# Performance work log

Measured on AMD Instinct MI355X. Metric: run time of the kernel, lower is better.

## Reference

```python
import jax, jax.numpy as jnp
import numpy as np

NUM_HEADS = 8
SPLIT = 2  # split_size; idx=0 -> H_sp=H, W_sp=SPLIT (horizontal stripes)


def setup_inputs() -> dict:
    key = jax.random.key(0)
    k1, k2, k3 = jax.random.split(key, 3)
    B, C, H, W = 4, 64, 128, 128
    temp = jax.random.normal(k1, (B, 3, C, H, W), dtype=jnp.float32)
    conv_w = jax.random.normal(k2, (C, 1, 3, 3), dtype=jnp.float32) * 0.1  # depthwise OIHW
    conv_b = jax.random.normal(k3, (C,), dtype=jnp.float32) * 0.1
    return {"temp": temp, "conv_w": conv_w, "conv_b": conv_b}


def reference(temp, conv_w, conv_b):
    B, _, C, H, W = temp.shape
    hd = C // NUM_HEADS
    scale = hd ** (-0.5)
    H_sp, W_sp = H, SPLIT  # idx == 0

    # symmetric pad to multiples of window size (faithful to original; zero here)
    H_pad = (H_sp - H % H_sp) % H_sp
    W_pad = (W_sp - W % W_sp) % W_sp
    top, left = H_pad // 2, W_pad // 2
    x = jnp.pad(temp, ((0, 0), (0, 0), (0, 0), (top, H_pad - top), (left, W_pad - left)))
    H_, W_ = H + H_pad, W + W_pad
    q, k, v = x[:, 0], x[:, 1], x[:, 2]  # each [B,C,H_,W_]

    nW = (H_ // H_sp) * (W_ // W_sp)
    N = H_sp * W_sp  # tokens per window

    def im2cswin(t):
        # [B,C,H_,W_] -> [B*nW, heads, N, hd]
        w = t.reshape(B, C, H_ // H_sp, H_sp, W_ // W_sp, W_sp)
        w = w.transpose(0, 2, 4, 3, 5, 1).reshape(-1, N, C)
        return w.reshape(-1, N, NUM_HEADS, hd).transpose(0, 2, 1, 3)

    qh = im2cswin(q) * scale
    kh = im2cswin(k)

    # v windows as images [B*nW, C, H_sp, W_sp] for depthwise LePE conv
    vw = v.reshape(B, C, H_ // H_sp, H_sp, W_ // W_sp, W_sp)
    vw = vw.transpose(0, 2, 4, 1, 3, 5).reshape(-1, C, H_sp, W_sp)
    rpe = jax.lax.conv_general_dilated(
        vw, conv_w, window_strides=(1, 1), padding='SAME',
        feature_group_count=C, dimension_numbers=('NCHW', 'OIHW', 'NCHW'))
    rpe = rpe + conv_b[None, :, None, None]

    vh = vw.reshape(-1, NUM_HEADS, hd, N).transpose(0, 1, 3, 2)    # [B*nW,h,N,hd]
    rpeh = rpe.reshape(-1, NUM_HEADS, hd, N).transpose(0, 1, 3, 2)

    attn = jax.nn.softmax(jnp.einsum('whnd,whmd->whnm', qh, kh), axis=-1)
    out = jnp.einsum('whnm,whmd->whnd', attn, vh) + rpeh           # [B*nW,h,N,hd]

    out = out.transpose(0, 2, 1, 3).reshape(-1, N, C)              # [B*nW,N,C]
    # windows2img + crop
    out = out.reshape(B, H_ // H_sp, W_ // W_sp, H_sp, W_sp, C)
    out = out.transpose(0, 1, 3, 2, 4, 5).reshape(B, H_, W_, C)
    out = out[:, top:H + top, left:W + left, :]
    return out.reshape(B, H * W, C)
```

## Files before the change

### kernel.cpp

```cpp
#include <hip/hip_runtime.h>
#include <hip/hip_bf16.h>
#include <stdint.h>


typedef __attribute__((ext_vector_type(4))) short bf16x4;
typedef __attribute__((ext_vector_type(4))) float f32x4;

static __device__ __forceinline__ uint32_t pk2(float x, float y) {
    union { __hip_bfloat162 h2; uint32_t u; } c;
    c.h2 = __float22bfloat162_rn(make_float2(x, y));
    return c.u;
}
static __device__ __forceinline__ float bflo(uint32_t u){ return __uint_as_float(u<<16); }
static __device__ __forceinline__ float bfhi(uint32_t u){ return __uint_as_float(u & 0xffff0000u); }

static __device__ __forceinline__ uint2 ld2(const char* p) {
    uint2 r;
    r.x = *(const uint32_t*)(p);
    r.y = *(const uint32_t*)(p + 4);
    return r;
}

static __device__ __forceinline__ int qk_off(int tok) {
    return (tok * 16) ^ ((tok >> 4 & 7) << 4);
}

static __device__ __forceinline__ f32x4 mfma16x16x16bf16(bf16x4 a, bf16x4 b, f32x4 c) {
#if __has_builtin(__builtin_amdgcn_mfma_f32_16x16x16bf16_1k)
    return __builtin_amdgcn_mfma_f32_16x16x16bf16_1k(a, b, c, 0, 0, 0);
#else
    f32x4 d;
    asm volatile("v_mfma_f32_16x16x16_bf16 %0, %1, %2, %3\n\ts_nop 7\n\ts_nop 7"
                 : "=v"(d) : "v"(a), "v"(b), "v"(c));
    return d;
#endif
}

#define QK_WIN_STR 4128
#define V_CH_STR   536
#define V_WIN_STR  4288

__global__ __launch_bounds__(256, 4)
void lepe_attn(const float* __restrict__ temp,
               const float* __restrict__ conv_w,
               const float* __restrict__ conv_b,
               float* __restrict__ out)
{
    __shared__ __align__(16) char smem[25408];
    char* q_s = smem;
    char* k_s = smem + 8256;
    char* v_t = smem + 16512;
    float* cw_s = (float*)(smem + 25088);

    const int tid  = threadIdx.x;
    const int wave = tid >> 6, lane = tid & 63;
    const int lr = lane & 15, quad = lane >> 4;
    const int win   = wave & 1;
    const int qbase = (wave >> 1) * 8;

    const int bid = blockIdx.x;
    const int x  = bid & 7;
    int t_ = bid >> 3;
    const int wq   = t_ & 3;  t_ >>= 2;
    const int head = t_ & 7;
    const int b    = t_ >> 3;
    const int wi   = x*8 + wq*2 + win;

    const size_t cstr = 16384, sstr = 64 * cstr;
    const float qs = 0.35355339059327373f * 1.4426950408889634f;

    {
        #pragma unroll
        for (int i = 0; i < 4; ++i) {
            int r  = i*256 + tid;
            int ch = r >> 7;
            int h  = r & 127;
            const float* bp = temp + (size_t)b*3*sstr + (size_t)(head*8 + ch)*cstr
                            + (size_t)h*128 + x*16 + wq*4;
            int o0 = qk_off(2*h), o1 = qk_off(2*h + 1);
            float4 fq = *(const float4*)(bp);
            uint32_t a0 = pk2(fq.x*qs, fq.y*qs);
            uint32_t a1 = pk2(fq.z*qs, fq.w*qs);
            *(uint16_t*)(q_s + o0 + ch*2)              = (uint16_t)a0;
            *(uint16_t*)(q_s + o1 + ch*2)              = (uint16_t)(a0>>16);
            *(uint16_t*)(q_s + QK_WIN_STR + o0 + ch*2) = (uint16_t)a1;
            *(uint16_t*)(q_s + QK_WIN_STR + o1 + ch*2) = (uint16_t)(a1>>16);
            float4 fk = *(const float4*)(bp + sstr);
            uint32_t b0 = pk2(fk.x, fk.y);
            uint32_t b1 = pk2(fk.z, fk.w);
            *(uint16_t*)(k_s + o0 + ch*2)              = (uint16_t)b0;
            *(uint16_t*)(k_s + o1 + ch*2)              = (uint16_t)(b0>>16);
            *(uint16_t*)(k_s + QK_WIN_STR + o0 + ch*2) = (uint16_t)b1;
            *(uint16_t*)(k_s + QK_WIN_STR + o1 + ch*2) = (uint16_t)(b1>>16);
            float4 fv = *(const float4*)(bp + 2*sstr);
            *(uint32_t*)(v_t + ch*V_CH_STR + 4*h + 4)             = pk2(fv.x, fv.y);
            *(uint32_t*)(v_t + V_WIN_STR + ch*V_CH_STR + 4*h + 4) = pk2(fv.z, fv.w);
        }
        if (tid < 72) cw_s[tid] = conv_w[head*72 + tid];
        if (tid < 8)  cw_s[72 + tid] = conv_b[head*8 + tid];
        if (tid < 16) {
            int vw = tid >> 3, vc = tid & 7;
            *(uint32_t*)(v_t + vw*V_WIN_STR + vc*V_CH_STR)       = 0;
            *(uint32_t*)(v_t + vw*V_WIN_STR + vc*V_CH_STR + 516) = 0;
        }
    }
    __syncthreads();

    const f32x4 zf = {0.f, 0.f, 0.f, 0.f};
    const uint2 z2 = make_uint2(0, 0);
    const uint2 ones2 = make_uint2(0x3F803F80u, 0x3F803F80u);
    uint2 kf[16]; uint2 vf[16];
    #pragma unroll
    for (int T = 0; T < 16; ++T) {
        uint2 kk = ld2(k_s + win*QK_WIN_STR + qk_off(T*16 + lr) + (quad & 1)*8);
        kf[T] = (quad < 2) ? kk : z2;
        uint2 vv = ld2(v_t + win*V_WIN_STR + (lane & 7)*V_CH_STR + 4 + (T*16 + quad*4)*2);
        vf[T] = (lr < 8) ? vv : ((lr == 8) ? ones2 : z2);
    }
    __syncthreads();

    {
        const int w2  = tid >> 7;
        const int chl = (tid >> 4) & 7;
        const int seg = tid & 15;
        const char* base = v_t + w2*V_WIN_STR + chl*V_CH_STR + seg*32;
        uint32_t d[10];
        *(uint2*)(d+0) = *(const uint2*)(base);
        *(uint2*)(d+2) = *(const uint2*)(base+8);
        *(uint2*)(d+4) = *(const uint2*)(base+16);
        *(uint2*)(d+6) = *(const uint2*)(base+24);
        *(uint2*)(d+8) = *(const uint2*)(base+32);
        float w9[9];
        #pragma unroll
        for (int k = 0; k < 9; ++k) w9[k] = cw_s[chl*9 + k];
        const float bia = cw_s[72 + chl];
        #pragma unroll
        for (int tt = 0; tt < 16; ++tt) {
            int tok = seg*16 + tt;
            int w01 = tok & 1;
            int L = (tt >> 1) * 2;
            float rp = bia;
            #pragma unroll
            for (int dy = 0; dy < 3; ++dy) {
                #pragma unroll
                for (int wp = 0; wp < 2; ++wp) {
                    int idx = L + 2*dy + wp;
                    uint32_t dw = d[idx >> 1];
                    float tap = (idx & 1) ? bfhi(dw) : bflo(dw);
                    rp = fmaf(w9[dy*3 + wp + 1 - w01], tap, rp);
                }
            }
            union { __hip_bfloat16 h; uint16_t u; } cv;
            cv.h = __float2bfloat16(rp);
            *(uint16_t*)(k_s + w2*QK_WIN_STR + qk_off(tok) + chl*2) = cv.u;
        }
    }
    __syncthreads();

    #pragma unroll 1
    for (int qg0 = 0; qg0 < 8; ++qg0) {
        const int qg = qbase + qg0;
        uint2 qq = ld2(q_s + win*QK_WIN_STR + qk_off(qg*16 + lr) + (quad & 1)*8);
        union { uint2 u; bf16x4 h4; } qf; qf.u = (quad < 2) ? qq : z2;
        f32x4 acc0 = zf, acc1 = zf;
        #pragma unroll
        for (int T = 0; T < 16; T += 2) {
            union { uint2 u; bf16x4 h4; } kfu0; kfu0.u = kf[T];
            union { uint2 u; bf16x4 h4; } kfu1; kfu1.u = kf[T+1];
            f32x4 sc0 = mfma16x16x16bf16(kfu0.h4, qf.h4, zf);
            f32x4 sc1 = mfma16x16x16bf16(kfu1.h4, qf.h4, zf);
            float a0 = __builtin_amdgcn_exp2f(sc0[0]);
            float a1 = __builtin_amdgcn_exp2f(sc0[1]);
            float a2 = __builtin_amdgcn_exp2f(sc0[2]);
            float a3 = __builtin_amdgcn_exp2f(sc0[3]);
            float b0_ = __builtin_amdgcn_exp2f(sc1[0]);
            float b1_ = __builtin_amdgcn_exp2f(sc1[1]);
            float b2_ = __builtin_amdgcn_exp2f(sc1[2]);
            float b3_ = __builtin_amdgcn_exp2f(sc1[3]);
            union { uint2 u; bf16x4 h4; } pb0; pb0.u = make_uint2(pk2(a0,a1), pk2(a2,a3));
            union { uint2 u; bf16x4 h4; } pb1; pb1.u = make_uint2(pk2(b0_,b1_), pk2(b2_,b3_));
            union { uint2 u; bf16x4 h4; } vf0; vf0.u = vf[T];
            union { uint2 u; bf16x4 h4; } vf1; vf1.u = vf[T+1];
            acc0 = mfma16x16x16bf16(vf0.h4, pb0.h4, acc0);
            acc1 = mfma16x16x16bf16(vf1.h4, pb1.h4, acc1);
        }
        f32x4 acc;
        acc[0] = acc0[0] + acc1[0];
        acc[1] = acc0[1] + acc1[1];
        acc[2] = acc0[2] + acc1[2];
        acc[3] = acc0[3] + acc1[3];
        float rs = __shfl(acc[0], 32 + lr);
        const float rinv = __builtin_amdgcn_rcpf(rs);
        if (quad < 2) {
            int tok = qg*16 + lr;
            int h = tok >> 1, w01 = tok & 1;
            uint2 rp2 = ld2(k_s + win*QK_WIN_STR + qk_off(tok) + quad*8);
            float4 ov;
            ov.x = fmaf(acc[0], rinv, bflo(rp2.x));
            ov.y = fmaf(acc[1], rinv, bfhi(rp2.x));
            ov.z = fmaf(acc[2], rinv, bflo(rp2.y));
            ov.w = fmaf(acc[3], rinv, bfhi(rp2.y));
            size_t addr = (size_t)b*1048576 + (size_t)(h*128 + wi*2 + w01)*64
                        + head*8 + quad*4;
            *(float4*)(out + addr) = ov;
        }
    }
}

extern "C" void kernel_launch(void* const* d_in, const int* in_sizes, int n_in,
                              void* d_out, int out_size, void* d_ws, size_t ws_size,
                              hipStream_t stream) {
    const float* temp = (const float*)d_in[0];
    const float* cw   = (const float*)d_in[1];
    const float* cb   = (const float*)d_in[2];
    float* o = (float*)d_out;
    (void)in_sizes; (void)n_in; (void)out_size; (void)d_ws; (void)ws_size;
    lepe_attn<<<dim3(1024), dim3(256), 0, stream>>>(temp, cw, cb, o);
}
```

Baseline: 112.8 us.

## Process eight windows per 1024-thread block for coalesced input loads

Each block now covers all eight stripe windows of a 16-column slab with 1024 threads and 100 KB of LDS, instead of two windows with 256 threads. Four consecutive threads read 64 contiguous bytes of a row, replacing the earlier 16-byte fragments, so global read coalescing should improve. The grid shrinks to 256 blocks, which allows only one block per CU because of the LDS size, and barriers now span 16 waves. The launch bound of 1024 threads with 4 blocks may also push the compiler into a tight register cap, which risks spilling the kf/vf fragment arrays.

```diff
diff --git a/kernel.cpp b/kernel.cpp
--- a/kernel.cpp
+++ b/kernel.cpp
@@ -40,65 +40,66 @@
 #define V_CH_STR   536
 #define V_WIN_STR  4288
 
-__global__ __launch_bounds__(256, 4)
+__global__ __launch_bounds__(1024, 4)
 void lepe_attn(const float* __restrict__ temp,
                const float* __restrict__ conv_w,
                const float* __restrict__ conv_b,
                float* __restrict__ out)
 {
-    __shared__ __align__(16) char smem[25408];
+    __shared__ __align__(16) char smem[100672];
     char* q_s = smem;
-    char* k_s = smem + 8256;
-    char* v_t = smem + 16512;
-    float* cw_s = (float*)(smem + 25088);
+    char* k_s = smem + 33024;
+    char* v_t = smem + 66048;
+    float* cw_s = (float*)(smem + 100352);
 
     const int tid  = threadIdx.x;
     const int wave = tid >> 6, lane = tid & 63;
     const int lr = lane & 15, quad = lane >> 4;
-    const int win   = wave & 1;
-    const int qbase = (wave >> 1) * 8;
+    const int win   = wave & 7;
+    const int qbase = (wave >> 3) * 8;
 
     const int bid = blockIdx.x;
-    const int x  = bid & 7;
+    const int x    = bid & 7;
     int t_ = bid >> 3;
-    const int wq   = t_ & 3;  t_ >>= 2;
     const int head = t_ & 7;
     const int b    = t_ >> 3;
-    const int wi   = x*8 + wq*2 + win;
+    const int wi   = x*8 + win;
 
     const size_t cstr = 16384, sstr = 64 * cstr;
     const float qs = 0.35355339059327373f * 1.4426950408889634f;
 
     {
+        const int chunk = tid & 3;
+        const int h     = (tid >> 2) & 127;
+        const int chp   = tid >> 9;
+        const int w0    = chunk * 2;
         #pragma unroll
         for (int i = 0; i < 4; ++i) {
-            int r  = i*256 + tid;
-            int ch = r >> 7;
-            int h  = r & 127;
+            int ch = i*2 + chp;
             const float* bp = temp + (size_t)b*3*sstr + (size_t)(head*8 + ch)*cstr
-                            + (size_t)h*128 + x*16 + wq*4;
+                            + (size_t)h*128 + x*16 + chunk*4;
             int o0 = qk_off(2*h), o1 = qk_off(2*h + 1);
             float4 fq = *(const float4*)(bp);
             uint32_t a0 = pk2(fq.x*qs, fq.y*qs);
             uint32_t a1 = pk2(fq.z*qs, fq.w*qs);
-            *(uint16_t*)(q_s + o0 + ch*2)              = (uint16_t)a0;
-            *(uint16_t*)(q_s + o1 + ch*2)              = (uint16_t)(a0>>16);
-            *(uint16_t*)(q_s + QK_WIN_STR + o0 + ch*2) = (uint16_t)a1;
-            *(uint16_t*)(q_s + QK_WIN_STR + o1 + ch*2) = (uint16_t)(a1>>16);
+            *(uint16_t*)(q_s + w0*QK_WIN_STR     + o0 + ch*2) = (uint16_t)a0;
+            *(uint16_t*)(q_s + w0*QK_WIN_STR     + o1 + ch*2) = (uint16_t)(a0>>16);
+            *(uint16_t*)(q_s + (w0+1)*QK_WIN_STR + o0 + ch*2) = (uint16_t)a1;
+            *(uint16_t*)(q_s + (w0+1)*QK_WIN_STR + o1 + ch*2) = (uint16_t)(a1>>16);
             float4 fk = *(const float4*)(bp + sstr);
             uint32_t b0 = pk2(fk.x, fk.y);
             uint32_t b1 = pk2(fk.z, fk.w);
-            *(uint16_t*)(k_s + o0 + ch*2)              = (uint16_t)b0;
-            *(uint16_t*)(k_s + o1 + ch*2)              = (uint16_t)(b0>>16);
-            *(uint16_t*)(k_s + QK_WIN_STR + o0 + ch*2) = (uint16_t)b1;
-            *(uint16_t*)(k_s + QK_WIN_STR + o1 + ch*2) = (uint16_t)(b1>>16);
+            *(uint16_t*)(k_s + w0*QK_WIN_STR     + o0 + ch*2) = (uint16_t)b0;
+            *(uint16_t*)(k_s + w0*QK_WIN_STR     + o1 + ch*2) = (uint16_t)(b0>>16);
+            *(uint16_t*)(k_s + (w0+1)*QK_WIN_STR + o0 + ch*2) = (uint16_t)b1;
+            *(uint16_t*)(k_s + (w0+1)*QK_WIN_STR + o1 + ch*2) = (uint16_t)(b1>>16);
             float4 fv = *(const float4*)(bp + 2*sstr);
-            *(uint32_t*)(v_t + ch*V_CH_STR + 4*h + 4)             = pk2(fv.x, fv.y);
-            *(uint32_t*)(v_t + V_WIN_STR + ch*V_CH_STR + 4*h + 4) = pk2(fv.z, fv.w);
+            *(uint32_t*)(v_t + w0*V_WIN_STR     + ch*V_CH_STR + 4*h + 4) = pk2(fv.x, fv.y);
+            *(uint32_t*)(v_t + (w0+1)*V_WIN_STR + ch*V_CH_STR + 4*h + 4) = pk2(fv.z, fv.w);
         }
         if (tid < 72) cw_s[tid] = conv_w[head*72 + tid];
         if (tid < 8)  cw_s[72 + tid] = conv_b[head*8 + tid];
-        if (tid < 16) {
+        if (tid < 64) {
             int vw = tid >> 3, vc = tid & 7;
             *(uint32_t*)(v_t + vw*V_WIN_STR + vc*V_CH_STR)       = 0;
             *(uint32_t*)(v_t + vw*V_WIN_STR + vc*V_CH_STR + 516) = 0;
@@ -215,5 +216,5 @@
     const float* cb   = (const float*)d_in[2];
     float* o = (float*)d_out;
     (void)in_sizes; (void)n_in; (void)out_size; (void)d_ws; (void)ws_size;
-    lepe_attn<<<dim3(1024), dim3(256), 0, stream>>>(temp, cw, cb, o);
-}
+    lepe_attn<<<dim3(256), dim3(1024), 0, stream>>>(temp, cw, cb, o);
+}
```

Result: slower. 118.8 us (+5.3%).
